# Optimization experiments

Measured on AMD Instinct MI355X. Metric: run time of the kernel, lower is better.

The kernel has to match this reference:

```python
import jax, jax.numpy as jnp
import numpy as np
from jax import lax

B, S, H = 2, 2048, 768
FF = 1536
E = 8
TOP_K = 2


def setup_inputs() -> dict:
    key = jax.random.key(0)
    k1, k2, k3, k4 = jax.random.split(key, 4)
    hidden_states = jax.random.normal(k1, (B, S, H), dtype=jnp.float32)
    # torch init: weight.normal_() for experts; nn.Linear default init for gate (approx normal here is fine for a numerics baseline)
    gate_w = jax.random.normal(k2, (E, H), dtype=jnp.float32) * 0.02
    w_fc = jax.random.normal(k3, (E, FF, H), dtype=jnp.float32) * 0.02
    w_proj = jax.random.normal(k4, (E, H, FF), dtype=jnp.float32) * 0.02
    return {"hidden_states": hidden_states, "gate_w": gate_w, "w_fc": w_fc, "w_proj": w_proj}


def reference(hidden_states, gate_w, w_fc, w_proj):
    b, s, h = hidden_states.shape
    x = hidden_states.reshape(-1, h)                      # [T, H]
    # --- top-k gating (logits in float32, as in the torch code) ---
    logits = (x @ gate_w.T).astype(jnp.float32)           # [T, E]
    top_logits, top_idx = lax.top_k(logits, TOP_K)        # [T, K]
    gates = jax.nn.softmax(top_logits, axis=1).astype(x.dtype)  # [T, K]
    # combined per-token/per-expert gate: g[t,e] = sum_k gates[t,k]*[idx[t,k]==e]
    onehot = jax.nn.one_hot(top_idx, E, dtype=x.dtype)    # [T, K, E]
    g = jnp.einsum('tk,tke->te', gates, onehot)           # [T, E]
    # --- experts: gather + per-expert GEMM + gated scatter-add combine ---
    # Equivalent math: tokens with zero gate for expert e contribute nothing,
    # so compute each expert on all tokens and weight by g[:, e].
    out = jnp.zeros_like(x)
    for e in range(E):  # fixed small loop over experts (structurally distinct weights)
        hmid = jax.nn.gelu(x @ w_fc[e].T, approximate=False)   # [T, FF] (torch gelu = erf form)
        out = out + g[:, e:e + 1] * (hmid @ w_proj[e].T)       # [T, H]
    out = out.reshape(b, s, h)
    return out, logits
```

## Files before the change

kernel.cpp:

```cpp
#include <hip/hip_runtime.h>
#include <hip/hip_bf16.h>
#include <math.h>
#include <stdint.h>

#define TOKENS 4096
#define HDIM   768
#define FFDIM  1536
#define NEXP   8

typedef __attribute__((ext_vector_type(8))) short bf16x8;
typedef __attribute__((ext_vector_type(4))) float f32x4;

__device__ __forceinline__ unsigned short f2bf(float f) {
    union { float f; uint32_t u; } c; c.f = f;
    uint32_t u = c.u;
    uint32_t r = (u + 0x7FFFu + ((u >> 16) & 1u)) >> 16;
    return (unsigned short)r;
}

__device__ __forceinline__ void gload_lds16(const void* g, void* l) {
    __builtin_amdgcn_global_load_lds(
        (const __attribute__((address_space(1))) void*)g,
        (__attribute__((address_space(3))) void*)l, 16, 0, 0);
}

__device__ __forceinline__ void cast4(const float* __restrict__ s,
                                      unsigned short* __restrict__ d, int i) {
    float4 v = ((const float4*)s)[i];
    ushort4 o;
    o.x = f2bf(v.x); o.y = f2bf(v.y); o.z = f2bf(v.z); o.w = f2bf(v.w);
    ((ushort4*)d)[i] = o;
}

__global__ __launch_bounds__(256) void gating(
    const float* __restrict__ x, const float* __restrict__ gw,
    float* __restrict__ logits,
    int* __restrict__ tok_e, float* __restrict__ tok_g,
    unsigned short* __restrict__ x_bf, float* __restrict__ outp)
{
    float4 zz = make_float4(0.f, 0.f, 0.f, 0.f);
#pragma unroll
    for (int j = 0; j < 3; j++)
        ((float4*)outp)[blockIdx.x * 768 + j * 256 + threadIdx.x] = zz;

    int t = blockIdx.x * 4 + (threadIdx.x >> 6);
    int lane = threadIdx.x & 63;
    const float4* xt = (const float4*)(x + (size_t)t * HDIM);
    const float4* gw4 = (const float4*)gw;
    ushort4* xbt = (ushort4*)(x_bf + (size_t)t * HDIM);
    float acc[NEXP];
#pragma unroll
    for (int e = 0; e < NEXP; e++) acc[e] = 0.f;
#pragma unroll
    for (int it = 0; it < 3; it++) {
        int i = lane + it * 64;
        float4 xv = xt[i];
        ushort4 o;
        o.x = f2bf(xv.x); o.y = f2bf(xv.y); o.z = f2bf(xv.z); o.w = f2bf(xv.w);
        xbt[i] = o;
#pragma unroll
        for (int e = 0; e < NEXP; e++) {
            float4 wv = gw4[e * 192 + i];
            acc[e] += xv.x * wv.x + xv.y * wv.y + xv.z * wv.z + xv.w * wv.w;
        }
    }
#pragma unroll
    for (int e = 0; e < NEXP; e++) {
#pragma unroll
        for (int off = 32; off > 0; off >>= 1)
            acc[e] += __shfl_xor(acc[e], off);
    }
    if (lane == 0) {
        float4 l0 = make_float4(acc[0], acc[1], acc[2], acc[3]);
        float4 l1 = make_float4(acc[4], acc[5], acc[6], acc[7]);
        float4* lp = (float4*)(logits + (size_t)t * NEXP);
        lp[0] = l0; lp[1] = l1;
        int i0 = 0; float v0 = acc[0];
#pragma unroll
        for (int e = 1; e < NEXP; e++) if (acc[e] > v0) { v0 = acc[e]; i0 = e; }
        int i1 = -1; float v1 = -3.4e38f;
#pragma unroll
        for (int e = 0; e < NEXP; e++) if (e != i0 && acc[e] > v1) { v1 = acc[e]; i1 = e; }
        float g0 = 1.f / (1.f + expf(v1 - v0));
        tok_e[t * 2] = i0; tok_e[t * 2 + 1] = i1;
        tok_g[t * 2] = g0; tok_g[t * 2 + 1] = 1.f - g0;
    }
}

__global__ __launch_bounds__(1024) void build_cast(
    const int* __restrict__ tok_e, const float* __restrict__ tok_g,
    int* __restrict__ counts,
    int* __restrict__ entries, float* __restrict__ gates,
    const float* __restrict__ wfc, unsigned short* __restrict__ wfc_bf, int n4)
{
    if (blockIdx.x >= 8) {
        int stride = 1024 * 1024;
        for (int i = (int)(blockIdx.x - 8) * 1024 + threadIdx.x; i < n4; i += stride)
            cast4(wfc, wfc_bf, i);
        return;
    }
    int e = blockIdx.x;
    __shared__ unsigned wtot[16], wbase[16];
    int tid = threadIdx.x;
    int lane = tid & 63, wid = tid >> 6;

    int eL[8]; float gL[8];
    int4 ea = ((const int4*)tok_e)[tid * 2];
    int4 eb = ((const int4*)tok_e)[tid * 2 + 1];
    float4 ga = ((const float4*)tok_g)[tid * 2];
    float4 gb = ((const float4*)tok_g)[tid * 2 + 1];
    eL[0] = ea.x; eL[1] = ea.y; eL[2] = ea.z; eL[3] = ea.w;
    eL[4] = eb.x; eL[5] = eb.y; eL[6] = eb.z; eL[7] = eb.w;
    gL[0] = ga.x; gL[1] = ga.y; gL[2] = ga.z; gL[3] = ga.w;
    gL[4] = gb.x; gL[5] = gb.y; gL[6] = gb.z; gL[7] = gb.w;

    unsigned m = 0, cnt = 0;
#pragma unroll
    for (int j = 0; j < 8; j++)
        if (eL[j] == e) { m |= 1u << j; cnt++; }

    unsigned il = cnt;
#pragma unroll
    for (int s = 1; s < 64; s <<= 1) {
        unsigned t1 = __shfl_up(il, s);
        if (lane >= s) il += t1;
    }
    if (lane == 63) wtot[wid] = il;
    __syncthreads();
    if (tid == 0) {
        unsigned r = 0;
#pragma unroll
        for (int i = 0; i < 16; i++) { unsigned a = wtot[i]; wbase[i] = r; r += a; }
        counts[e] = (int)r;
    }
    __syncthreads();
    unsigned slot = wbase[wid] + (il - cnt);
#pragma unroll
    for (int j = 0; j < 8; j++) {
        if (m & (1u << j)) {
            entries[e * TOKENS + slot] = tid * 8 + j;
            gates[e * TOKENS + slot]   = gL[j];
            slot++;
        }
    }
}

template<int KD, int ND, int TN, int NCTP, int GG, bool IS_FC, bool DBUF>
__global__ __launch_bounds__(512) void moe_gemm(
    const unsigned short* __restrict__ Asrc,
    const unsigned short* __restrict__ Bsrc,
    const int* __restrict__ counts,
    const int* __restrict__ entries,
    const float* __restrict__ gates,
    unsigned short* __restrict__ hmid,
    float* __restrict__ outp,
    const float* __restrict__ castS, unsigned short* __restrict__ castD, int castN4)
{
    if constexpr (IS_FC) {
        if (blockIdx.x >= GG) {
            int stride = 512 * 512;
            for (int i = (int)(blockIdx.x - GG) * 512 + threadIdx.x; i < castN4; i += stride)
                cast4(castS, castD, i);
            return;
        }
    }
    constexpr int BM = 256;
    constexpr int SLOTS = GG / 8;
    constexpr int AJ = TN / 32;
    constexpr int CB = TN / 64;
    constexpr int NV = 4 + CB;
    int bkt  = blockIdx.x & 7;
    int slot = blockIdx.x >> 3;

    int n_e = counts[bkt];
    int rts = (n_e + BM - 1) >> 8;
    int nfill = rts * NCTP;
    if (slot >= nfill) return;
    int ebase = 0;
#pragma unroll
    for (int e = 0; e < NEXP; e++) { int c = counts[e]; if (e < bkt) ebase += c; }
    const int* lst = entries + bkt * TOKENS;

    int tid = threadIdx.x;
    int w = tid >> 6;
    int l = tid & 63;
    int sg = l & 7;
    int lr8 = l >> 3;
    int lo = l & 15;
    int q  = l >> 4;
    int wr = w >> 1, wc = w & 1;

    __shared__ __align__(16) unsigned short sA[(DBUF ? 2 : 1) * BM * 64];
    __shared__ __align__(16) unsigned short sB[(DBUF ? 2 : 1) * TN * 64];
    unsigned short* sA0 = sA;
    unsigned short* sA1 = sA + BM * 64;
    unsigned short* sB0 = sB;
    unsigned short* sB1 = sB + TN * 64;

    int aOff[4][2], bOff[AJ][2];
#pragma unroll
    for (int i = 0; i < 4; i++) {
        int m = wr * 64 + i * 16 + lo;
#pragma unroll
        for (int s = 0; s < 2; s++)
            aOff[i][s] = m * 64 + ((s * 4 + q) ^ (m & 7)) * 8;
    }
#pragma unroll
    for (int j = 0; j < AJ; j++) {
        int n = wc * (TN / 2) + j * 16 + lo;
#pragma unroll
        for (int s = 0; s < 2; s++)
            bOff[j][s] = n * 64 + ((s * 4 + q) ^ (n & 7)) * 8;
    }

    for (int p = slot; p < nfill; p += SLOTS) {
        int ct   = p / rts;
        int r    = p - ct * rts;
        int row0 = r << 8;
        int n0 = ct * TN;

        const unsigned short* Ag[4];
        int aLds[4];
#pragma unroll
        for (int c = 0; c < 4; c++) {
            int rr = w * 32 + c * 8 + lr8;
            int gr = row0 + rr;
            int id = gr < n_e ? gr : n_e - 1;
            size_t arow = IS_FC ? (size_t)(lst[id] >> 1) : (size_t)(ebase + id);
            Ag[c] = Asrc + arow * KD + (size_t)((sg ^ (rr & 7)) * 8);
            aLds[c] = (w * 32 + c * 8) * 64;
        }
        const unsigned short* Bg[CB];
        int bLds[CB];
#pragma unroll
        for (int c = 0; c < CB; c++) {
            int rr = w * (TN / 8) + c * 8 + lr8;
            Bg[c] = Bsrc + ((size_t)bkt * ND + n0 + rr) * KD + (size_t)((sg ^ (rr & 7)) * 8);
            bLds[c] = (w * (TN / 8) + c * 8) * 64;
        }

        f32x4 acc[4][AJ];
#pragma unroll
        for (int i = 0; i < 4; i++)
#pragma unroll
            for (int j = 0; j < AJ; j++) acc[i][j] = (f32x4){0.f, 0.f, 0.f, 0.f};

        auto stage = [&](unsigned short* SA, unsigned short* SB, int k0) {
#pragma unroll
            for (int c = 0; c < 4; c++) gload_lds16(Ag[c] + k0, SA + aLds[c]);
#pragma unroll
            for (int c = 0; c < CB; c++) gload_lds16(Bg[c] + k0, SB + bLds[c]);
        };
        auto compute = [&](const unsigned short* SA, const unsigned short* SB) {
#pragma unroll
            for (int s = 0; s < 2; s++) {
                bf16x8 a[4], b[AJ];
#pragma unroll
                for (int i = 0; i < 4; i++) a[i] = *(const bf16x8*)(SA + aOff[i][s]);
#pragma unroll
                for (int j = 0; j < AJ; j++) b[j] = *(const bf16x8*)(SB + bOff[j][s]);
#pragma unroll
                for (int i = 0; i < 4; i++)
#pragma unroll
                    for (int j = 0; j < AJ; j++)
                        acc[i][j] = __builtin_amdgcn_mfma_f32_16x16x32_bf16(a[i], b[j], acc[i][j], 0, 0, 0);
            }
        };

        if constexpr (!DBUF) {
            for (int k0 = 0; k0 < KD; k0 += 64) {
                stage(sA0, sB0, k0);
                __syncthreads();
                compute(sA0, sB0);
                __syncthreads();
            }
        } else {
#define WAITN asm volatile("s_waitcnt vmcnt(%0)" :: "n"(NV) : "memory")
#define WAIT0 asm volatile("s_waitcnt vmcnt(0)" ::: "memory")
            stage(sA0, sB0, 0);
            for (int k0 = 0; k0 < KD; k0 += 128) {
                stage(sA1, sB1, k0 + 64);
                WAITN;
                __builtin_amdgcn_s_barrier();
                __builtin_amdgcn_s_setprio(1);
                compute(sA0, sB0);
                __builtin_amdgcn_s_setprio(0);
                __builtin_amdgcn_s_barrier();
                if (k0 + 128 < KD) {
                    stage(sA0, sB0, k0 + 128);
                    WAITN;
                } else {
                    WAIT0;
                }
                __builtin_amdgcn_s_barrier();
                __builtin_amdgcn_s_setprio(1);
                compute(sA1, sB1);
                __builtin_amdgcn_s_setprio(0);
                __builtin_amdgcn_s_barrier();
            }
#undef WAITN
#undef WAIT0
        }

#pragma unroll
        for (int i = 0; i < 4; i++) {
            int rowB = row0 + wr * 64 + i * 16 + q * 4;
#pragma unroll
            for (int rr = 0; rr < 4; rr++) {
                int orow = rowB + rr;
                if (orow < n_e) {
                    if (IS_FC) {
                        size_t hrow = (size_t)(ebase + orow);
#pragma unroll
                        for (int j = 0; j < AJ; j++) {
                            float v = acc[i][j][rr];
                            v = 0.5f * v * (1.f + erff(v * 0.70710678118654752f));
                            hmid[hrow * ND + n0 + wc * (TN / 2) + j * 16 + lo] = f2bf(v);
                        }
                    } else {
                        int token = lst[orow] >> 1;
                        float g = gates[bkt * TOKENS + orow];
#pragma unroll
                        for (int j = 0; j < AJ; j++) {
                            atomicAdd(&outp[(size_t)token * ND + n0 + wc * (TN / 2) + j * 16 + lo],
                                      acc[i][j][rr] * g);
                        }
                    }
                }
            }
        }
    }
}

extern "C" void kernel_launch(void* const* d_in, const int* in_sizes, int n_in,
                              void* d_out, int out_size, void* d_ws, size_t ws_size,
                              hipStream_t stream) {
    const float* x     = (const float*)d_in[0];
    const float* gw    = (const float*)d_in[1];
    const float* wfc   = (const float*)d_in[2];
    const float* wproj = (const float*)d_in[3];
    float* outp   = (float*)d_out;
    float* logits = outp + (size_t)TOKENS * HDIM;

    char* ws = (char*)d_ws;
    int*   counts  = (int*)ws;
    size_t off = 256;
    int*   entries = (int*)(ws + off);
    float* gates   = (float*)(ws + off + NEXP * TOKENS * 4);
    off += 2ull * NEXP * TOKENS * 4;
    int*   tok_e   = (int*)(ws + off);   off += (size_t)TOKENS * 2 * 4;
    float* tok_g   = (float*)(ws + off); off += (size_t)TOKENS * 2 * 4;
    unsigned short* x_bf   = (unsigned short*)(ws + off); off += (size_t)TOKENS * HDIM * 2;
    unsigned short* wfc_bf = (unsigned short*)(ws + off); off += (size_t)NEXP * FFDIM * HDIM * 2;
    unsigned short* wpj_bf = (unsigned short*)(ws + off); off += (size_t)NEXP * HDIM * FFDIM * 2;
    unsigned short* hmid   = (unsigned short*)(ws + off);

    gating<<<TOKENS / 4, 256, 0, stream>>>(x, gw, logits, tok_e, tok_g, x_bf, outp);
    build_cast<<<8 + 1024, 1024, 0, stream>>>(tok_e, tok_g, counts, entries, gates,
                                              wfc, wfc_bf, NEXP * FFDIM * HDIM / 4);
    moe_gemm<HDIM, FFDIM, 128, FFDIM / 128, 768, true,  false>
        <<<768 + 512, 512, 0, stream>>>(
        x_bf, wfc_bf, counts, entries, gates, hmid, outp,
        wproj, wpj_bf, NEXP * HDIM * FFDIM / 4);
    moe_gemm<FFDIM, HDIM, 64,  HDIM / 64,   512, false, true >
        <<<512, 512, 0, stream>>>(
        hmid, wpj_bf, counts, entries, gates, hmid, outp,
        nullptr, nullptr, 0);
}
```

Measured before the change: 215.0 us.

## Fold routing scan into FC GEMM and move w_fc cast into gating

```diff
diff --git a/kernel.cpp b/kernel.cpp
--- a/kernel.cpp
+++ b/kernel.cpp
@@ -10,6 +10,8 @@
 
 typedef __attribute__((ext_vector_type(8))) short bf16x8;
 typedef __attribute__((ext_vector_type(4))) float f32x4;
+typedef __attribute__((ext_vector_type(4))) float fvec4;
+typedef __attribute__((ext_vector_type(4))) unsigned short usvec4;
 
 __device__ __forceinline__ unsigned short f2bf(float f) {
     union { float f; uint32_t u; } c; c.f = f;
@@ -24,20 +26,29 @@
         (__attribute__((address_space(3))) void*)l, 16, 0, 0);
 }
 
+template<bool NTST>
 __device__ __forceinline__ void cast4(const float* __restrict__ s,
                                       unsigned short* __restrict__ d, int i) {
-    float4 v = ((const float4*)s)[i];
-    ushort4 o;
+    fvec4 v = __builtin_nontemporal_load((const fvec4*)s + i);
+    usvec4 o;
     o.x = f2bf(v.x); o.y = f2bf(v.y); o.z = f2bf(v.z); o.w = f2bf(v.w);
-    ((ushort4*)d)[i] = o;
+    if constexpr (NTST) __builtin_nontemporal_store(o, (usvec4*)d + i);
+    else                ((usvec4*)d)[i] = o;
 }
 
 __global__ __launch_bounds__(256) void gating(
     const float* __restrict__ x, const float* __restrict__ gw,
     float* __restrict__ logits,
     int* __restrict__ tok_e, float* __restrict__ tok_g,
-    unsigned short* __restrict__ x_bf, float* __restrict__ outp)
+    unsigned short* __restrict__ x_bf, float* __restrict__ outp,
+    const float* __restrict__ wfc, unsigned short* __restrict__ wfc_bf, int n4)
 {
+    if (blockIdx.x >= 1024) {
+        int stride = 1024 * 256;
+        for (int i = (int)(blockIdx.x - 1024) * 256 + threadIdx.x; i < n4; i += stride)
+            cast4<false>(wfc, wfc_bf, i);
+        return;
+    }
     float4 zz = make_float4(0.f, 0.f, 0.f, 0.f);
 #pragma unroll
     for (int j = 0; j < 3; j++)
@@ -87,80 +98,23 @@
     }
 }
 
-__global__ __launch_bounds__(1024) void build_cast(
-    const int* __restrict__ tok_e, const float* __restrict__ tok_g,
-    int* __restrict__ counts,
-    int* __restrict__ entries, float* __restrict__ gates,
-    const float* __restrict__ wfc, unsigned short* __restrict__ wfc_bf, int n4)
-{
-    if (blockIdx.x >= 8) {
-        int stride = 1024 * 1024;
-        for (int i = (int)(blockIdx.x - 8) * 1024 + threadIdx.x; i < n4; i += stride)
-            cast4(wfc, wfc_bf, i);
-        return;
-    }
-    int e = blockIdx.x;
-    __shared__ unsigned wtot[16], wbase[16];
-    int tid = threadIdx.x;
-    int lane = tid & 63, wid = tid >> 6;
-
-    int eL[8]; float gL[8];
-    int4 ea = ((const int4*)tok_e)[tid * 2];
-    int4 eb = ((const int4*)tok_e)[tid * 2 + 1];
-    float4 ga = ((const float4*)tok_g)[tid * 2];
-    float4 gb = ((const float4*)tok_g)[tid * 2 + 1];
-    eL[0] = ea.x; eL[1] = ea.y; eL[2] = ea.z; eL[3] = ea.w;
-    eL[4] = eb.x; eL[5] = eb.y; eL[6] = eb.z; eL[7] = eb.w;
-    gL[0] = ga.x; gL[1] = ga.y; gL[2] = ga.z; gL[3] = ga.w;
-    gL[4] = gb.x; gL[5] = gb.y; gL[6] = gb.z; gL[7] = gb.w;
-
-    unsigned m = 0, cnt = 0;
-#pragma unroll
-    for (int j = 0; j < 8; j++)
-        if (eL[j] == e) { m |= 1u << j; cnt++; }
-
-    unsigned il = cnt;
-#pragma unroll
-    for (int s = 1; s < 64; s <<= 1) {
-        unsigned t1 = __shfl_up(il, s);
-        if (lane >= s) il += t1;
-    }
-    if (lane == 63) wtot[wid] = il;
-    __syncthreads();
-    if (tid == 0) {
-        unsigned r = 0;
-#pragma unroll
-        for (int i = 0; i < 16; i++) { unsigned a = wtot[i]; wbase[i] = r; r += a; }
-        counts[e] = (int)r;
-    }
-    __syncthreads();
-    unsigned slot = wbase[wid] + (il - cnt);
-#pragma unroll
-    for (int j = 0; j < 8; j++) {
-        if (m & (1u << j)) {
-            entries[e * TOKENS + slot] = tid * 8 + j;
-            gates[e * TOKENS + slot]   = gL[j];
-            slot++;
-        }
-    }
-}
-
-template<int KD, int ND, int TN, int NCTP, int GG, bool IS_FC, bool DBUF>
+template<int KD, int ND, int TN, int NCTP, int GG, bool IS_FC, bool DBUF, bool SCAN>
 __global__ __launch_bounds__(512) void moe_gemm(
     const unsigned short* __restrict__ Asrc,
     const unsigned short* __restrict__ Bsrc,
-    const int* __restrict__ counts,
-    const int* __restrict__ entries,
-    const float* __restrict__ gates,
+    int* __restrict__ counts,
+    int* __restrict__ entries,
+    float* __restrict__ gates,
     unsigned short* __restrict__ hmid,
     float* __restrict__ outp,
-    const float* __restrict__ castS, unsigned short* __restrict__ castD, int castN4)
+    const float* __restrict__ castS, unsigned short* __restrict__ castD, int castN4,
+    const int* __restrict__ tok_e, const float* __restrict__ tok_g)
 {
     if constexpr (IS_FC) {
         if (blockIdx.x >= GG) {
             int stride = 512 * 512;
             for (int i = (int)(blockIdx.x - GG) * 512 + threadIdx.x; i < castN4; i += stride)
-                cast4(castS, castD, i);
+                cast4<true>(castS, castD, i);
             return;
         }
     }
@@ -171,17 +125,60 @@
     constexpr int NV = 4 + CB;
     int bkt  = blockIdx.x & 7;
     int slot = blockIdx.x >> 3;
-
-    int n_e = counts[bkt];
+    int tid = threadIdx.x;
+
+    __shared__ unsigned long long swlo[SCAN ? 8 : 1], swhi[SCAN ? 8 : 1];
+    __shared__ int s_cnt[SCAN ? 8 : 1];
+    __shared__ int s_lst[SCAN ? 256 : 1];
+
+    int n_e, ebase;
+    if constexpr (SCAN) {
+        int lane = tid & 63, wid = tid >> 6;
+        unsigned long long clo = 0, chi = 0;
+#pragma unroll
+        for (int b = 0; b < 4; b++) {
+            int4 ev = ((const int4*)tok_e)[tid * 4 + b];
+            int e4[4] = {ev.x, ev.y, ev.z, ev.w};
+#pragma unroll
+            for (int j = 0; j < 4; j++) {
+                unsigned long long one = 1ull << ((e4[j] & 3) * 16);
+                if (e4[j] < 4) clo += one; else chi += one;
+            }
+        }
+#pragma unroll
+        for (int s = 1; s < 64; s <<= 1) {
+            clo += __shfl_xor(clo, s);
+            chi += __shfl_xor(chi, s);
+        }
+        if (lane == 0) { swlo[wid] = clo; swhi[wid] = chi; }
+        __syncthreads();
+        if (tid == 0) {
+            unsigned long long rl = 0, rh = 0;
+#pragma unroll
+            for (int i = 0; i < 8; i++) { rl += swlo[i]; rh += swhi[i]; }
+#pragma unroll
+            for (int e = 0; e < 4; e++) {
+                s_cnt[e]     = (int)((rl >> (e * 16)) & 0xFFFF);
+                s_cnt[e + 4] = (int)((rh >> (e * 16)) & 0xFFFF);
+            }
+        }
+        __syncthreads();
+        n_e = s_cnt[bkt];
+        if (slot == 0 && tid == 0) counts[bkt] = n_e;
+        ebase = 0;
+#pragma unroll
+        for (int e = 0; e < NEXP; e++) if (e < bkt) ebase += s_cnt[e];
+    } else {
+        n_e = counts[bkt];
+        ebase = 0;
+#pragma unroll
+        for (int e = 0; e < NEXP; e++) { int c = counts[e]; if (e < bkt) ebase += c; }
+    }
     int rts = (n_e + BM - 1) >> 8;
     int nfill = rts * NCTP;
     if (slot >= nfill) return;
-    int ebase = 0;
-#pragma unroll
-    for (int e = 0; e < NEXP; e++) { int c = counts[e]; if (e < bkt) ebase += c; }
     const int* lst = entries + bkt * TOKENS;
 
-    int tid = threadIdx.x;
     int w = tid >> 6;
     int l = tid & 63;
     int sg = l & 7;
@@ -219,6 +216,64 @@
         int row0 = r << 8;
         int n0 = ct * TN;
 
+        if constexpr (SCAN) {
+            int lane = tid & 63, wid = tid >> 6;
+            int eL[16]; float gL[16];
+#pragma unroll
+            for (int b = 0; b < 4; b++) {
+                int4 ev = ((const int4*)tok_e)[tid * 4 + b];
+                float4 gv = ((const float4*)tok_g)[tid * 4 + b];
+                eL[b*4+0] = ev.x; eL[b*4+1] = ev.y; eL[b*4+2] = ev.z; eL[b*4+3] = ev.w;
+                gL[b*4+0] = gv.x; gL[b*4+1] = gv.y; gL[b*4+2] = gv.z; gL[b*4+3] = gv.w;
+            }
+            unsigned long long clo = 0, chi = 0;
+#pragma unroll
+            for (int j = 0; j < 16; j++) {
+                unsigned long long one = 1ull << ((eL[j] & 3) * 16);
+                if (eL[j] < 4) clo += one; else chi += one;
+            }
+            unsigned long long ilo = clo, ihi = chi;
+#pragma unroll
+            for (int s = 1; s < 64; s <<= 1) {
+                unsigned long long t1 = __shfl_up(ilo, s);
+                unsigned long long t2 = __shfl_up(ihi, s);
+                if (lane >= s) { ilo += t1; ihi += t2; }
+            }
+            __syncthreads();
+            if (lane == 63) { swlo[wid] = ilo; swhi[wid] = ihi; }
+            __syncthreads();
+            if (tid == 0) {
+                unsigned long long rl = 0, rh = 0;
+#pragma unroll
+                for (int i = 0; i < 8; i++) {
+                    unsigned long long a = swlo[i], b2 = swhi[i];
+                    swlo[i] = rl; swhi[i] = rh;
+                    rl += a; rh += b2;
+                }
+            }
+            __syncthreads();
+            unsigned long long rlo = swlo[wid] + (ilo - clo);
+            unsigned long long rhi = swhi[wid] + (ihi - chi);
+#pragma unroll
+            for (int j = 0; j < 16; j++) {
+                int e = eL[j];
+                int sh = (e & 3) * 16;
+                unsigned long long one = 1ull << sh;
+                int sv;
+                if (e < 4) { sv = (int)((rlo >> sh) & 0xFFFF); rlo += one; }
+                else       { sv = (int)((rhi >> sh) & 0xFFFF); rhi += one; }
+                if (e == bkt) {
+                    int rel = sv - row0;
+                    if ((unsigned)rel < 256u) s_lst[rel] = tid * 16 + j;
+                    if (p == 0) {
+                        entries[bkt * TOKENS + sv] = tid * 16 + j;
+                        gates[bkt * TOKENS + sv]   = gL[j];
+                    }
+                }
+            }
+            __syncthreads();
+        }
+
         const unsigned short* Ag[4];
         int aLds[4];
 #pragma unroll
@@ -226,7 +281,9 @@
             int rr = w * 32 + c * 8 + lr8;
             int gr = row0 + rr;
             int id = gr < n_e ? gr : n_e - 1;
-            size_t arow = IS_FC ? (size_t)(lst[id] >> 1) : (size_t)(ebase + id);
+            size_t arow;
+            if constexpr (IS_FC) arow = (size_t)(s_lst[id - row0] >> 1);
+            else                 arow = (size_t)(ebase + id);
             Ag[c] = Asrc + arow * KD + (size_t)((sg ^ (rr & 7)) * 8);
             aLds[c] = (w * 32 + c * 8) * 64;
         }
@@ -355,15 +412,16 @@
     unsigned short* wpj_bf = (unsigned short*)(ws + off); off += (size_t)NEXP * HDIM * FFDIM * 2;
     unsigned short* hmid   = (unsigned short*)(ws + off);
 
-    gating<<<TOKENS / 4, 256, 0, stream>>>(x, gw, logits, tok_e, tok_g, x_bf, outp);
-    build_cast<<<8 + 1024, 1024, 0, stream>>>(tok_e, tok_g, counts, entries, gates,
-                                              wfc, wfc_bf, NEXP * FFDIM * HDIM / 4);
-    moe_gemm<HDIM, FFDIM, 128, FFDIM / 128, 768, true,  false>
+    gating<<<2048, 256, 0, stream>>>(x, gw, logits, tok_e, tok_g, x_bf, outp,
+                                     wfc, wfc_bf, NEXP * FFDIM * HDIM / 4);
+    moe_gemm<HDIM, FFDIM, 128, FFDIM / 128, 768, true,  false, true>
         <<<768 + 512, 512, 0, stream>>>(
         x_bf, wfc_bf, counts, entries, gates, hmid, outp,
-        wproj, wpj_bf, NEXP * HDIM * FFDIM / 4);
-    moe_gemm<FFDIM, HDIM, 64,  HDIM / 64,   512, false, true >
+        wproj, wpj_bf, NEXP * HDIM * FFDIM / 4,
+        tok_e, tok_g);
+    moe_gemm<FFDIM, HDIM, 64,  HDIM / 64,   512, false, true, false>
         <<<512, 512, 0, stream>>>(
         hmid, wpj_bf, counts, entries, gates, hmid, outp,
-        nullptr, nullptr, 0);
-}
+        nullptr, nullptr, 0,
+        nullptr, nullptr);
+}
```

After: 235.5 us. 1.1x slower.

## Fuse MoE pipeline into one cooperative persistent kernel with grid syncs

Applied to the files above, without the earlier changes.

```diff
diff --git a/kernel.cpp b/kernel.cpp
--- a/kernel.cpp
+++ b/kernel.cpp
@@ -1,15 +1,21 @@
 #include <hip/hip_runtime.h>
+#include <hip/hip_cooperative_groups.h>
 #include <hip/hip_bf16.h>
 #include <math.h>
 #include <stdint.h>
+
+namespace cg = cooperative_groups;
 
 #define TOKENS 4096
 #define HDIM   768
 #define FFDIM  1536
 #define NEXP   8
+#define N4W    (NEXP * FFDIM * HDIM / 4)
 
 typedef __attribute__((ext_vector_type(8))) short bf16x8;
 typedef __attribute__((ext_vector_type(4))) float f32x4;
+typedef __attribute__((ext_vector_type(4))) float fvec4;
+typedef __attribute__((ext_vector_type(4))) unsigned short usvec4;
 
 __device__ __forceinline__ unsigned short f2bf(float f) {
     union { float f; uint32_t u; } c; c.f = f;
@@ -24,101 +30,30 @@
         (__attribute__((address_space(3))) void*)l, 16, 0, 0);
 }
 
+template<bool NTST>
 __device__ __forceinline__ void cast4(const float* __restrict__ s,
                                       unsigned short* __restrict__ d, int i) {
-    float4 v = ((const float4*)s)[i];
-    ushort4 o;
+    fvec4 v = __builtin_nontemporal_load((const fvec4*)s + i);
+    usvec4 o;
     o.x = f2bf(v.x); o.y = f2bf(v.y); o.z = f2bf(v.z); o.w = f2bf(v.w);
-    ((ushort4*)d)[i] = o;
-}
-
-__global__ __launch_bounds__(256) void gating(
-    const float* __restrict__ x, const float* __restrict__ gw,
-    float* __restrict__ logits,
-    int* __restrict__ tok_e, float* __restrict__ tok_g,
-    unsigned short* __restrict__ x_bf, float* __restrict__ outp)
+    if constexpr (NTST) __builtin_nontemporal_store(o, (usvec4*)d + i);
+    else                ((usvec4*)d)[i] = o;
+}
+
+__device__ void scan_expert(int e,
+    const int* __restrict__ tok_e, const float* __restrict__ tok_g,
+    int* __restrict__ counts, int* __restrict__ entries, float* __restrict__ gates,
+    unsigned* wtot, unsigned* wbase)
 {
-    float4 zz = make_float4(0.f, 0.f, 0.f, 0.f);
-#pragma unroll
-    for (int j = 0; j < 3; j++)
-        ((float4*)outp)[blockIdx.x * 768 + j * 256 + threadIdx.x] = zz;
-
-    int t = blockIdx.x * 4 + (threadIdx.x >> 6);
-    int lane = threadIdx.x & 63;
-    const float4* xt = (const float4*)(x + (size_t)t * HDIM);
-    const float4* gw4 = (const float4*)gw;
-    ushort4* xbt = (ushort4*)(x_bf + (size_t)t * HDIM);
-    float acc[NEXP];
-#pragma unroll
-    for (int e = 0; e < NEXP; e++) acc[e] = 0.f;
-#pragma unroll
-    for (int it = 0; it < 3; it++) {
-        int i = lane + it * 64;
-        float4 xv = xt[i];
-        ushort4 o;
-        o.x = f2bf(xv.x); o.y = f2bf(xv.y); o.z = f2bf(xv.z); o.w = f2bf(xv.w);
-        xbt[i] = o;
-#pragma unroll
-        for (int e = 0; e < NEXP; e++) {
-            float4 wv = gw4[e * 192 + i];
-            acc[e] += xv.x * wv.x + xv.y * wv.y + xv.z * wv.z + xv.w * wv.w;
-        }
-    }
-#pragma unroll
-    for (int e = 0; e < NEXP; e++) {
-#pragma unroll
-        for (int off = 32; off > 0; off >>= 1)
-            acc[e] += __shfl_xor(acc[e], off);
-    }
-    if (lane == 0) {
-        float4 l0 = make_float4(acc[0], acc[1], acc[2], acc[3]);
-        float4 l1 = make_float4(acc[4], acc[5], acc[6], acc[7]);
-        float4* lp = (float4*)(logits + (size_t)t * NEXP);
-        lp[0] = l0; lp[1] = l1;
-        int i0 = 0; float v0 = acc[0];
-#pragma unroll
-        for (int e = 1; e < NEXP; e++) if (acc[e] > v0) { v0 = acc[e]; i0 = e; }
-        int i1 = -1; float v1 = -3.4e38f;
-#pragma unroll
-        for (int e = 0; e < NEXP; e++) if (e != i0 && acc[e] > v1) { v1 = acc[e]; i1 = e; }
-        float g0 = 1.f / (1.f + expf(v1 - v0));
-        tok_e[t * 2] = i0; tok_e[t * 2 + 1] = i1;
-        tok_g[t * 2] = g0; tok_g[t * 2 + 1] = 1.f - g0;
-    }
-}
-
-__global__ __launch_bounds__(1024) void build_cast(
-    const int* __restrict__ tok_e, const float* __restrict__ tok_g,
-    int* __restrict__ counts,
-    int* __restrict__ entries, float* __restrict__ gates,
-    const float* __restrict__ wfc, unsigned short* __restrict__ wfc_bf, int n4)
-{
-    if (blockIdx.x >= 8) {
-        int stride = 1024 * 1024;
-        for (int i = (int)(blockIdx.x - 8) * 1024 + threadIdx.x; i < n4; i += stride)
-            cast4(wfc, wfc_bf, i);
-        return;
-    }
-    int e = blockIdx.x;
-    __shared__ unsigned wtot[16], wbase[16];
-    int tid = threadIdx.x;
-    int lane = tid & 63, wid = tid >> 6;
-
-    int eL[8]; float gL[8];
-    int4 ea = ((const int4*)tok_e)[tid * 2];
-    int4 eb = ((const int4*)tok_e)[tid * 2 + 1];
-    float4 ga = ((const float4*)tok_g)[tid * 2];
-    float4 gb = ((const float4*)tok_g)[tid * 2 + 1];
-    eL[0] = ea.x; eL[1] = ea.y; eL[2] = ea.z; eL[3] = ea.w;
-    eL[4] = eb.x; eL[5] = eb.y; eL[6] = eb.z; eL[7] = eb.w;
-    gL[0] = ga.x; gL[1] = ga.y; gL[2] = ga.z; gL[3] = ga.w;
-    gL[4] = gb.x; gL[5] = gb.y; gL[6] = gb.z; gL[7] = gb.w;
-
-    unsigned m = 0, cnt = 0;
-#pragma unroll
-    for (int j = 0; j < 8; j++)
-        if (eL[j] == e) { m |= 1u << j; cnt++; }
-
+    int tid = threadIdx.x, lane = tid & 63, wid = tid >> 6;
+    const int4* te4 = (const int4*)tok_e;
+    const float4* tg4 = (const float4*)tok_g;
+    unsigned cnt = 0;
+#pragma unroll
+    for (int b = 0; b < 4; b++) {
+        int4 ev = te4[tid * 4 + b];
+        cnt += (ev.x == e) + (ev.y == e) + (ev.z == e) + (ev.w == e);
+    }
     unsigned il = cnt;
 #pragma unroll
     for (int s = 1; s < 64; s <<= 1) {
@@ -130,52 +65,49 @@
     if (tid == 0) {
         unsigned r = 0;
 #pragma unroll
-        for (int i = 0; i < 16; i++) { unsigned a = wtot[i]; wbase[i] = r; r += a; }
+        for (int i = 0; i < 8; i++) { unsigned a = wtot[i]; wbase[i] = r; r += a; }
         counts[e] = (int)r;
     }
     __syncthreads();
-    unsigned slot = wbase[wid] + (il - cnt);
-#pragma unroll
-    for (int j = 0; j < 8; j++) {
-        if (m & (1u << j)) {
-            entries[e * TOKENS + slot] = tid * 8 + j;
-            gates[e * TOKENS + slot]   = gL[j];
-            slot++;
-        }
-    }
-}
-
-template<int KD, int ND, int TN, int NCTP, int GG, bool IS_FC, bool DBUF>
-__global__ __launch_bounds__(512) void moe_gemm(
+    unsigned slot = wbase[wid] + il - cnt;
+#pragma unroll
+    for (int b = 0; b < 4; b++) {
+        int4 ev = te4[tid * 4 + b];
+        float4 gv = tg4[tid * 4 + b];
+        int ee[4] = {ev.x, ev.y, ev.z, ev.w};
+        float gg[4] = {gv.x, gv.y, gv.z, gv.w};
+#pragma unroll
+        for (int j = 0; j < 4; j++) {
+            if (ee[j] == e) {
+                entries[e * TOKENS + slot] = tid * 16 + b * 4 + j;
+                gates[e * TOKENS + slot]   = gg[j];
+                slot++;
+            }
+        }
+    }
+}
+
+template<int KD, int ND, int TN, int NCTP, bool IS_FC, bool DBUF>
+__device__ void gemm_phase(unsigned short* smem,
     const unsigned short* __restrict__ Asrc,
     const unsigned short* __restrict__ Bsrc,
     const int* __restrict__ counts,
     const int* __restrict__ entries,
     const float* __restrict__ gates,
     unsigned short* __restrict__ hmid,
-    float* __restrict__ outp,
-    const float* __restrict__ castS, unsigned short* __restrict__ castD, int castN4)
+    float* __restrict__ outp)
 {
-    if constexpr (IS_FC) {
-        if (blockIdx.x >= GG) {
-            int stride = 512 * 512;
-            for (int i = (int)(blockIdx.x - GG) * 512 + threadIdx.x; i < castN4; i += stride)
-                cast4(castS, castD, i);
-            return;
-        }
-    }
     constexpr int BM = 256;
-    constexpr int SLOTS = GG / 8;
     constexpr int AJ = TN / 32;
     constexpr int CB = TN / 64;
     constexpr int NV = 4 + CB;
-    int bkt  = blockIdx.x & 7;
-    int slot = blockIdx.x >> 3;
+    int slots = (int)(gridDim.x >> 3);
+    int bkt  = (int)(blockIdx.x & 7);
+    int slot = (int)(blockIdx.x >> 3);
 
     int n_e = counts[bkt];
     int rts = (n_e + BM - 1) >> 8;
     int nfill = rts * NCTP;
-    if (slot >= nfill) return;
     int ebase = 0;
 #pragma unroll
     for (int e = 0; e < NEXP; e++) { int c = counts[e]; if (e < bkt) ebase += c; }
@@ -190,12 +122,10 @@
     int q  = l >> 4;
     int wr = w >> 1, wc = w & 1;
 
-    __shared__ __align__(16) unsigned short sA[(DBUF ? 2 : 1) * BM * 64];
-    __shared__ __align__(16) unsigned short sB[(DBUF ? 2 : 1) * TN * 64];
-    unsigned short* sA0 = sA;
-    unsigned short* sA1 = sA + BM * 64;
-    unsigned short* sB0 = sB;
-    unsigned short* sB1 = sB + TN * 64;
+    unsigned short* sA0 = smem;
+    unsigned short* sA1 = smem + BM * 64;
+    unsigned short* sB0 = DBUF ? (smem + 2 * BM * 64) : (smem + BM * 64);
+    unsigned short* sB1 = DBUF ? (smem + 2 * BM * 64 + TN * 64) : (smem + BM * 64);
 
     int aOff[4][2], bOff[AJ][2];
 #pragma unroll
@@ -213,7 +143,7 @@
             bOff[j][s] = n * 64 + ((s * 4 + q) ^ (n & 7)) * 8;
     }
 
-    for (int p = slot; p < nfill; p += SLOTS) {
+    for (int p = slot; p < nfill; p += slots) {
         int ct   = p / rts;
         int r    = p - ct * rts;
         int row0 = r << 8;
@@ -332,6 +262,94 @@
     }
 }
 
+struct MoeP {
+    const float *x, *gw, *wfc, *wproj;
+    float *outp, *logits;
+    int *counts, *entries;
+    float *gates;
+    int *tok_e; float *tok_g;
+    unsigned short *x_bf, *wfc_bf, *wpj_bf, *hmid;
+};
+
+__global__ __launch_bounds__(512, 4) void moe_fused(MoeP P)
+{
+    __shared__ __align__(16) unsigned short smem[40960];
+    cg::grid_group grid = cg::this_grid();
+    int tid = threadIdx.x, bid = (int)blockIdx.x, nb = (int)gridDim.x;
+
+    float4 zz = make_float4(0.f, 0.f, 0.f, 0.f);
+    for (int i = bid * 512 + tid; i < TOKENS * HDIM / 4; i += nb * 512)
+        ((float4*)P.outp)[i] = zz;
+
+    {
+        int lane = tid & 63, w = tid >> 6;
+        for (int tg = bid; tg < TOKENS / 8; tg += nb) {
+            int t = tg * 8 + w;
+            const float4* xt = (const float4*)(P.x + (size_t)t * HDIM);
+            const float4* gw4 = (const float4*)P.gw;
+            ushort4* xbt = (ushort4*)(P.x_bf + (size_t)t * HDIM);
+            float acc[NEXP];
+#pragma unroll
+            for (int e = 0; e < NEXP; e++) acc[e] = 0.f;
+#pragma unroll
+            for (int it = 0; it < 3; it++) {
+                int i = lane + it * 64;
+                float4 xv = xt[i];
+                ushort4 o;
+                o.x = f2bf(xv.x); o.y = f2bf(xv.y); o.z = f2bf(xv.z); o.w = f2bf(xv.w);
+                xbt[i] = o;
+#pragma unroll
+                for (int e = 0; e < NEXP; e++) {
+                    float4 wv = gw4[e * 192 + i];
+                    acc[e] += xv.x * wv.x + xv.y * wv.y + xv.z * wv.z + xv.w * wv.w;
+                }
+            }
+#pragma unroll
+            for (int e = 0; e < NEXP; e++) {
+#pragma unroll
+                for (int off = 32; off > 0; off >>= 1)
+                    acc[e] += __shfl_xor(acc[e], off);
+            }
+            if (lane == 0) {
+                float4 l0 = make_float4(acc[0], acc[1], acc[2], acc[3]);
+                float4 l1 = make_float4(acc[4], acc[5], acc[6], acc[7]);
+                float4* lp = (float4*)(P.logits + (size_t)t * NEXP);
+                lp[0] = l0; lp[1] = l1;
+                int i0 = 0; float v0 = acc[0];
+#pragma unroll
+                for (int e = 1; e < NEXP; e++) if (acc[e] > v0) { v0 = acc[e]; i0 = e; }
+                int i1 = -1; float v1 = -3.4e38f;
+#pragma unroll
+                for (int e = 0; e < NEXP; e++) if (e != i0 && acc[e] > v1) { v1 = acc[e]; i1 = e; }
+                float g0 = 1.f / (1.f + expf(v1 - v0));
+                P.tok_e[t * 2] = i0; P.tok_e[t * 2 + 1] = i1;
+                P.tok_g[t * 2] = g0; P.tok_g[t * 2 + 1] = 1.f - g0;
+            }
+        }
+    }
+    for (int i = bid * 512 + tid; i < N4W; i += nb * 512)
+        cast4<false>(P.wfc, P.wfc_bf, i);
+
+    __threadfence();
+    grid.sync();
+
+    if (bid < NEXP)
+        scan_expert(bid, P.tok_e, P.tok_g, P.counts, P.entries, P.gates,
+                    (unsigned*)smem, (unsigned*)smem + 8);
+    __threadfence();
+    grid.sync();
+
+    gemm_phase<HDIM, FFDIM, 128, FFDIM / 128, true, false>(
+        smem, P.x_bf, P.wfc_bf, P.counts, P.entries, P.gates, P.hmid, P.outp);
+    for (int i = bid * 512 + tid; i < N4W; i += nb * 512)
+        cast4<true>(P.wproj, P.wpj_bf, i);
+    __threadfence();
+    grid.sync();
+
+    gemm_phase<FFDIM, HDIM, 64, HDIM / 64, false, true>(
+        smem, P.hmid, P.wpj_bf, P.counts, P.entries, P.gates, P.hmid, P.outp);
+}
+
 extern "C" void kernel_launch(void* const* d_in, const int* in_sizes, int n_in,
                               void* d_out, int out_size, void* d_ws, size_t ws_size,
                               hipStream_t stream) {
@@ -355,15 +373,20 @@
     unsigned short* wpj_bf = (unsigned short*)(ws + off); off += (size_t)NEXP * HDIM * FFDIM * 2;
     unsigned short* hmid   = (unsigned short*)(ws + off);
 
-    gating<<<TOKENS / 4, 256, 0, stream>>>(x, gw, logits, tok_e, tok_g, x_bf, outp);
-    build_cast<<<8 + 1024, 1024, 0, stream>>>(tok_e, tok_g, counts, entries, gates,
-                                              wfc, wfc_bf, NEXP * FFDIM * HDIM / 4);
-    moe_gemm<HDIM, FFDIM, 128, FFDIM / 128, 768, true,  false>
-        <<<768 + 512, 512, 0, stream>>>(
-        x_bf, wfc_bf, counts, entries, gates, hmid, outp,
-        wproj, wpj_bf, NEXP * HDIM * FFDIM / 4);
-    moe_gemm<FFDIM, HDIM, 64,  HDIM / 64,   512, false, true >
-        <<<512, 512, 0, stream>>>(
-        hmid, wpj_bf, counts, entries, gates, hmid, outp,
-        nullptr, nullptr, 0);
-}
+    MoeP P;
+    P.x = x; P.gw = gw; P.wfc = wfc; P.wproj = wproj;
+    P.outp = outp; P.logits = logits;
+    P.counts = counts; P.entries = entries; P.gates = gates;
+    P.tok_e = tok_e; P.tok_g = tok_g;
+    P.x_bf = x_bf; P.wfc_bf = wfc_bf; P.wpj_bf = wpj_bf; P.hmid = hmid;
+
+    int maxB = 2;
+    (void)hipOccupancyMaxActiveBlocksPerMultiprocessor(&maxB, moe_fused, 512, 0);
+    int grid = maxB * 256;
+    if (grid > 512) grid = 512;
+    if (grid < 8)   grid = 256;
+
+    void* args[] = { (void*)&P };
+    (void)hipLaunchCooperativeKernel((const void*)moe_fused, dim3(grid), dim3(512),
+                                     args, 0, stream);
+}
```

After: 529.9 us. 2.47x slower.
